# Optimization experiments

Hardware: AMD Instinct MI355X
Metric: run time of the kernel (lower is better)

Reference implementation:

```python
import jax, jax.numpy as jnp
import numpy as np

N_NODES = 50000
N_EDGES = 500000
EDGE_DIM = 16
DIM = 128          # num_features == hidden == 128 so all layers share shapes
N_LAYERS = 3
N_GRAPHS = 512
N_CLASSES = 10
BN_EPS = 1e-5


def _bn(x, g, b, rm, rv):
    # eval-mode BatchNorm1d
    return (x - rm) * jax.lax.rsqrt(rv + BN_EPS) * g + b


def setup_inputs() -> dict:
    key = jax.random.key(0)
    ks = jax.random.split(key, 32)
    s = 0.05
    inp = {
        "x": jax.random.normal(ks[0], (N_NODES, DIM), jnp.float32),
        "edge_attr": jax.random.normal(ks[1], (N_EDGES, EDGE_DIM), jnp.float32),
        "edge_index": jax.random.randint(ks[2], (2, N_EDGES), 0, N_NODES, jnp.int64),
        "batch": jnp.sort(jax.random.randint(ks[3], (N_NODES,), 0, N_GRAPHS, jnp.int64)),
        # edge encoder params (stacked over layers)
        "ee_w1": jax.random.normal(ks[4], (N_LAYERS, EDGE_DIM, DIM), jnp.float32) * s,
        "ee_b1": jax.random.normal(ks[5], (N_LAYERS, DIM), jnp.float32) * s,
        "ee_w2": jax.random.normal(ks[6], (N_LAYERS, DIM, DIM), jnp.float32) * s,
        "ee_b2": jax.random.normal(ks[7], (N_LAYERS, DIM), jnp.float32) * s,
        "ee_bn_g": 1.0 + 0.1 * jax.random.normal(ks[8], (N_LAYERS, DIM), jnp.float32),
        "ee_bn_b": 0.1 * jax.random.normal(ks[9], (N_LAYERS, DIM), jnp.float32),
        "ee_bn_rm": 0.1 * jax.random.normal(ks[10], (N_LAYERS, DIM), jnp.float32),
        "ee_bn_rv": jax.random.uniform(ks[11], (N_LAYERS, DIM), jnp.float32, 0.5, 1.5),
        # node MLP params (stacked over layers)
        "mlp_w1": jax.random.normal(ks[12], (N_LAYERS, DIM, DIM), jnp.float32) * s,
        "mlp_b1": jax.random.normal(ks[13], (N_LAYERS, DIM), jnp.float32) * s,
        "mlp_w2": jax.random.normal(ks[14], (N_LAYERS, DIM, DIM), jnp.float32) * s,
        "mlp_b2": jax.random.normal(ks[15], (N_LAYERS, DIM), jnp.float32) * s,
        "mlp_bn_g": 1.0 + 0.1 * jax.random.normal(ks[16], (N_LAYERS, DIM), jnp.float32),
        "mlp_bn_b": 0.1 * jax.random.normal(ks[17], (N_LAYERS, DIM), jnp.float32),
        "mlp_bn_rm": 0.1 * jax.random.normal(ks[18], (N_LAYERS, DIM), jnp.float32),
        "mlp_bn_rv": jax.random.uniform(ks[19], (N_LAYERS, DIM), jnp.float32, 0.5, 1.5),
        # readout heads
        "lin1_w": jax.random.normal(ks[20], (DIM, DIM), jnp.float32) * s,
        "lin1_b": jax.random.normal(ks[21], (DIM,), jnp.float32) * s,
        "lin2_w": jax.random.normal(ks[22], (DIM, N_CLASSES), jnp.float32) * s,
        "lin2_b": jax.random.normal(ks[23], (N_CLASSES,), jnp.float32) * s,
    }
    return inp


def _forward(x, edge_attr, ee_w1, ee_b1, ee_w2, ee_b2, ee_bn_g, ee_bn_b, ee_bn_rm, ee_bn_rv,
             mlp_w1, mlp_b1, mlp_w2, mlp_b2, mlp_bn_g, mlp_bn_b, mlp_bn_rm, mlp_bn_rv,
             lin1_w, lin1_b, lin2_w, lin2_b, edge_index, batch):
    src, dst = edge_index[0], edge_index[1]  # x_j gathered from src, aggregated at dst
    n_nodes = x.shape[0]
    for i in range(N_LAYERS):
        # edge encoder: Linear -> ReLU -> Linear -> ReLU -> BN
        e = jax.nn.relu(edge_attr @ ee_w1[i] + ee_b1[i])
        e = jax.nn.relu(e @ ee_w2[i] + ee_b2[i])
        e = _bn(e, ee_bn_g[i], ee_bn_b[i], ee_bn_rm[i], ee_bn_rv[i])
        # message: relu(x_j + edge_emb), aggregate: scatter-add to dst
        msg = jax.nn.relu(x[src] + e)                         # [E, DIM]
        agg = jax.ops.segment_sum(msg, dst, num_segments=n_nodes)
        # mlp(x + agg): Linear -> ReLU -> Linear -> ReLU -> BN
        h = x + agg
        h = jax.nn.relu(h @ mlp_w1[i] + mlp_b1[i])
        h = jax.nn.relu(h @ mlp_w2[i] + mlp_b2[i])
        x = _bn(h, mlp_bn_g[i], mlp_bn_b[i], mlp_bn_rm[i], mlp_bn_rv[i])
    # global mean pool over graphs
    sums = jax.ops.segment_sum(x, batch, num_segments=N_GRAPHS)          # [G, DIM]
    cnts = jax.ops.segment_sum(jnp.ones((n_nodes, 1), x.dtype), batch, num_segments=N_GRAPHS)
    pooled = sums / jnp.maximum(cnts, 1.0)
    h = jax.nn.relu(pooled @ lin1_w + lin1_b)   # dropout off in eval mode
    logits = h @ lin2_w + lin2_b
    return jax.nn.log_softmax(logits, axis=-1)


def reference(x, edge_attr, ee_w1, ee_b1, ee_w2, ee_b2, ee_bn_g, ee_bn_b, ee_bn_rm, ee_bn_rv,
              mlp_w1, mlp_b1, mlp_w2, mlp_b2, mlp_bn_g, mlp_bn_b, mlp_bn_rm, mlp_bn_rv,
              lin1_w, lin1_b, lin2_w, lin2_b, edge_index, batch):
    return _forward(x, edge_attr, ee_w1, ee_b1, ee_w2, ee_b2, ee_bn_g, ee_bn_b, ee_bn_rm, ee_bn_rv,
                    mlp_w1, mlp_b1, mlp_w2, mlp_b2, mlp_bn_g, mlp_bn_b, mlp_bn_rm, mlp_bn_rv,
                    lin1_w, lin1_b, lin2_w, lin2_b, edge_index, batch)
```

## Files before the change

### kernel.cpp

```cpp
#include <hip/hip_runtime.h>

#define N_NODES_C 50000
#define N_EDGES_C 500000
#define EDGE_DIM_C 16
#define DIM_C 128
#define N_LAYERS_C 3
#define N_GRAPHS_C 512
#define N_CLASSES_C 10
#define BN_EPS_C 1e-5f

#define SCAN_NB ((N_NODES_C + 1023) / 1024)

typedef short bf16x8 __attribute__((ext_vector_type(8)));
typedef float f32x4  __attribute__((ext_vector_type(4)));

__device__ inline unsigned cvt_pk_bf16(float a, float b) {
    unsigned r;
    asm("v_cvt_pk_bf16_f32 %0, %1, %2" : "=v"(r) : "v"(a), "v"(b));
    return r;
}
__device__ inline float bf2f(unsigned short h) {
    union { unsigned u; float f; } v; v.u = ((unsigned)h) << 16;
    return v.f;
}

__global__ void hist_kernel(const int* __restrict__ dst, int* __restrict__ cnt)
{
    int e = blockIdx.x * blockDim.x + threadIdx.x;
    if (e < N_EDGES_C) atomicAdd(&cnt[dst[e]], 1);
}

__global__ __launch_bounds__(1024)
void scan1_kernel(const int* __restrict__ cnt, int* __restrict__ incl,
                  int* __restrict__ bsum)
{
    __shared__ int buf[1024];
    int i = blockIdx.x * 1024 + threadIdx.x;
    int v = (i < N_NODES_C) ? cnt[i] : 0;
    buf[threadIdx.x] = v;
    __syncthreads();
    for (int off = 1; off < 1024; off <<= 1) {
        int t = (threadIdx.x >= off) ? buf[threadIdx.x - off] : 0;
        __syncthreads();
        buf[threadIdx.x] += t;
        __syncthreads();
    }
    if (i < N_NODES_C) incl[i] = buf[threadIdx.x];
    if (threadIdx.x == 1023) bsum[blockIdx.x] = buf[1023];
}

__global__ void scan2_kernel(int* __restrict__ bsum)
{
    if (threadIdx.x == 0 && blockIdx.x == 0) {
        int run = 0;
        for (int b = 0; b < SCAN_NB; ++b) { int v = bsum[b]; bsum[b] = run; run += v; }
    }
}

__global__ __launch_bounds__(1024)
void scan3_kernel(const int* __restrict__ cnt, const int* __restrict__ incl,
                  const int* __restrict__ bsum,
                  int* __restrict__ offsets, int* __restrict__ cursor)
{
    int i = blockIdx.x * 1024 + threadIdx.x;
    if (i < N_NODES_C) {
        int inc = incl[i] + bsum[blockIdx.x];
        offsets[i + 1] = inc;
        cursor[i] = inc - cnt[i];
        if (i == 0) offsets[0] = 0;
    }
}

__global__ void scatter_kernel(const int* __restrict__ src,
                               const int* __restrict__ dst,
                               const float* __restrict__ ea,
                               int* __restrict__ cursor,
                               int* __restrict__ srcPerm,
                               unsigned short* __restrict__ eaPermH)
{
    int e = blockIdx.x * blockDim.x + threadIdx.x;
    if (e >= N_EDGES_C) return;
    int pos = atomicAdd(&cursor[dst[e]], 1);
    srcPerm[pos] = src[e];
    const float4* in = (const float4*)&ea[(size_t)e * EDGE_DIM_C];
    float4 a = in[0], b = in[1], c = in[2], d = in[3];
    uint4 lo, hi;
    lo.x = cvt_pk_bf16(a.x, a.y); lo.y = cvt_pk_bf16(a.z, a.w);
    lo.z = cvt_pk_bf16(b.x, b.y); lo.w = cvt_pk_bf16(b.z, b.w);
    hi.x = cvt_pk_bf16(c.x, c.y); hi.y = cvt_pk_bf16(c.z, c.w);
    hi.z = cvt_pk_bf16(d.x, d.y); hi.w = cvt_pk_bf16(d.z, d.w);
    uint4* outp = (uint4*)&eaPermH[(size_t)pos * EDGE_DIM_C];
    outp[0] = lo; outp[1] = hi;
}

__global__ __launch_bounds__(512)
void goff_kernel(const int* __restrict__ batch, int* __restrict__ goff)
{
    int g = threadIdx.x;
    int lo = 0, hi = N_NODES_C;
    while (lo < hi) {
        int mid = (lo + hi) >> 1;
        if (batch[mid] < g) lo = mid + 1; else hi = mid;
    }
    goff[g] = lo;
    if (g == 0) goff[N_GRAPHS_C] = N_NODES_C;
}

__global__ __launch_bounds__(256)
void wprep_kernel(const float* __restrict__ ee_w1, const float* __restrict__ ee_w2,
                  const float* __restrict__ mlp_w1, const float* __restrict__ mlp_w2,
                  short* __restrict__ W1T, short* __restrict__ W2T,
                  short* __restrict__ MT1, short* __restrict__ MT2)
{
    int b = blockIdx.x;
    int l = b % 3;
    int which = b / 3;
    if (which == 0) {
        const float* in = ee_w1 + l * 16 * 128;
        short* outp = W1T + l * 128 * 16;
        for (int i = threadIdx.x; i < 2048; i += 256) {
            int f = i >> 4, k = i & 15;
            outp[i] = (short)(cvt_pk_bf16(in[k * 128 + f], 0.f) & 0xffff);
        }
    } else {
        const float* in = (which == 1 ? ee_w2 : which == 2 ? mlp_w1 : mlp_w2) + l * 128 * 128;
        short* outp = (which == 1 ? W2T : which == 2 ? MT1 : MT2) + l * 128 * 128;
        for (int i = threadIdx.x; i < 16384; i += 256) {
            int f = i >> 7, k = i & 127;
            outp[i] = (short)(cvt_pk_bf16(in[k * 128 + f], 0.f) & 0xffff);
        }
    }
}

__global__ __launch_bounds__(256)
void emb_mfma(const unsigned short* __restrict__ eaPermH,
              const short* __restrict__ W1T, const float* __restrict__ b1,
              const short* __restrict__ W2T, const float* __restrict__ b2,
              const float* __restrict__ bng, const float* __restrict__ bnb,
              const float* __restrict__ bnrm, const float* __restrict__ bnrv,
              unsigned short* __restrict__ emb, int c0, int chunkN)
{
    __shared__ short t1s[64 * 128];

    const int tid  = threadIdx.x;
    const int lane = tid & 63;
    const int w    = tid >> 6;
    const int ln15 = lane & 15;
    const int g    = lane >> 4;
    const int colbase = w * 32;

    bf16x8 fw1[2], fw2[2][4];
    float b1v[2], b2v[2], scv[2], shv[2];
    #pragma unroll
    for (int ct = 0; ct < 2; ++ct) {
        int f = colbase + ct * 16 + ln15;
        if (g < 2) fw1[ct] = *(const bf16x8*)&W1T[f * 16 + g * 8];
        else       fw1[ct] = (bf16x8){0,0,0,0,0,0,0,0};
        #pragma unroll
        for (int kb = 0; kb < 4; ++kb)
            fw2[ct][kb] = *(const bf16x8*)&W2T[f * 128 + kb * 32 + g * 8];
        b1v[ct] = b1[f]; b2v[ct] = b2[f];
        float sc = bng[f] * rsqrtf(bnrv[f] + BN_EPS_C);
        scv[ct] = sc; shv[ct] = bnb[f] - bnrm[f] * sc;
    }

    const int niter = (chunkN + 63) / 64;
    for (int it = blockIdx.x; it < niter; it += gridDim.x) {
        const int eb = it * 64;

        #pragma unroll
        for (int rt = 0; rt < 4; ++rt) {
            bf16x8 af;
            if (g < 2) {
                int erow = min(eb + rt * 16 + ln15, chunkN - 1);
                af = *(const bf16x8*)&eaPermH[(size_t)(c0 + erow) * EDGE_DIM_C + g * 8];
            } else {
                af = (bf16x8){0,0,0,0,0,0,0,0};
            }
            #pragma unroll
            for (int ct = 0; ct < 2; ++ct) {
                f32x4 a1 = { b1v[ct], b1v[ct], b1v[ct], b1v[ct] };
                a1 = __builtin_amdgcn_mfma_f32_16x16x32_bf16(af, fw1[ct], a1, 0, 0, 0);
                int col = colbase + ct * 16 + ln15;
                #pragma unroll
                for (int r = 0; r < 4; ++r) {
                    int row = rt * 16 + g * 4 + r;
                    int idx = (row * 128 + col) ^ ((row & 15) << 3);
                    t1s[idx] = (short)(cvt_pk_bf16(fmaxf(a1[r], 0.f), 0.f) & 0xffff);
                }
            }
        }
        __syncthreads();

        f32x4 acc[4][2];
        #pragma unroll
        for (int rt = 0; rt < 4; ++rt)
            #pragma unroll
            for (int ct = 0; ct < 2; ++ct)
                acc[rt][ct] = (f32x4){ b2v[ct], b2v[ct], b2v[ct], b2v[ct] };

        #pragma unroll
        for (int rt = 0; rt < 4; ++rt) {
            bf16x8 a[4];
            int row = rt * 16 + ln15;
            #pragma unroll
            for (int kb = 0; kb < 4; ++kb) {
                int idx = (row * 128 + kb * 32 + g * 8) ^ ((row & 15) << 3);
                a[kb] = *(const bf16x8*)&t1s[idx];
            }
            #pragma unroll
            for (int ct = 0; ct < 2; ++ct)
                #pragma unroll
                for (int kb = 0; kb < 4; ++kb)
                    acc[rt][ct] = __builtin_amdgcn_mfma_f32_16x16x32_bf16(
                        a[kb], fw2[ct][kb], acc[rt][ct], 0, 0, 0);
        }
        __syncthreads();

        #pragma unroll
        for (int rt = 0; rt < 4; ++rt)
            #pragma unroll
            for (int ct = 0; ct < 2; ++ct) {
                int col = colbase + ct * 16 + ln15;
                #pragma unroll
                for (int r = 0; r < 4; ++r) {
                    int row = rt * 16 + g * 4 + r;
                    float v = fmaxf(acc[rt][ct][r], 0.f) * scv[ct] + shv[ct];
                    int idx = (row * 128 + col) ^ ((row & 15) << 3);
                    t1s[idx] = (short)(cvt_pk_bf16(v, 0.f) & 0xffff);
                }
            }
        __syncthreads();

        for (int i = tid; i < 1024; i += 256) {
            int row = i >> 4;
            int c8  = (i & 15) * 8;
            if (eb + row < chunkN) {
                int idx = (row * 128 + c8) ^ ((row & 15) << 3);
                bf16x8 v = *(const bf16x8*)&t1s[idx];
                *(bf16x8*)&emb[(size_t)(eb + row) * 128 + c8] = v;
            }
        }
        __syncthreads();
    }
}

__global__ __launch_bounds__(256)
void agg_kernel(const unsigned short* __restrict__ emb,
                const float* __restrict__ x,
                const int* __restrict__ srcPerm,
                const int* __restrict__ offsets,
                float* __restrict__ agg,
                int c0, int c1, int first)
{
    const int slot = threadIdx.x >> 5;
    const int l    = threadIdx.x & 31;
    const int n = blockIdx.x * 8 + slot;
    if (n >= N_NODES_C) return;

    int lo = offsets[n], hi = offsets[n + 1];
    lo = max(lo, c0); hi = min(hi, c1);

    float4 s = make_float4(0.f, 0.f, 0.f, 0.f);
    const bool any = lo < hi;
    for (int pos = lo; pos < hi; ++pos) {
        int srcn = srcPerm[pos];
        ushort4 eb = *(const ushort4*)&emb[(size_t)(pos - c0) * DIM_C + l * 4];
        float4 xv = *(const float4*)&x[(size_t)srcn * DIM_C + l * 4];
        s.x += fmaxf(xv.x + bf2f(eb.x), 0.f);
        s.y += fmaxf(xv.y + bf2f(eb.y), 0.f);
        s.z += fmaxf(xv.z + bf2f(eb.z), 0.f);
        s.w += fmaxf(xv.w + bf2f(eb.w), 0.f);
    }

    float4* ap = (float4*)&agg[(size_t)n * DIM_C + l * 4];
    if (first) {
        *ap = s;
    } else if (any) {
        float4 o = *ap;
        o.x += s.x; o.y += s.y; o.z += s.z; o.w += s.w;
        *ap = o;
    }
}

__global__ __launch_bounds__(256)
void node_fused(const float* __restrict__ in0, const float* __restrict__ in1,
                const short* __restrict__ WT1, const float* __restrict__ b1,
                const short* __restrict__ WT2, const float* __restrict__ b2,
                const float* __restrict__ bng, const float* __restrict__ bnb,
                const float* __restrict__ bnrm, const float* __restrict__ bnrv,
                float* __restrict__ out, int nrows)
{
    __shared__ short smem[2 * 64 * 128];
    short* hs  = smem;
    short* t1s = smem + 64 * 128;
    float* fout = (float*)smem;

    const int tid  = threadIdx.x;
    const int lane = tid & 63;
    const int w    = tid >> 6;
    const int ln15 = lane & 15;
    const int g    = lane >> 4;
    const int colbase = w * 32;

    bf16x8 fw1[2][4], fw2[2][4];
    float b1v[2], b2v[2], scv[2], shv[2];
    #pragma unroll
    for (int ct = 0; ct < 2; ++ct) {
        int f = colbase + ct * 16 + ln15;
        #pragma unroll
        for (int kb = 0; kb < 4; ++kb) {
            fw1[ct][kb] = *(const bf16x8*)&WT1[f * 128 + kb * 32 + g * 8];
            fw2[ct][kb] = *(const bf16x8*)&WT2[f * 128 + kb * 32 + g * 8];
        }
        b1v[ct] = b1[f]; b2v[ct] = b2[f];
        float sc = bng[f] * rsqrtf(bnrv[f] + BN_EPS_C);
        scv[ct] = sc; shv[ct] = bnb[f] - bnrm[f] * sc;
    }

    const int ntiles = (nrows + 63) / 64;
    for (int t = blockIdx.x; t < ntiles; t += gridDim.x) {
        const int base = t * 64;

        for (int i = tid; i < 2048; i += 256) {
            int row = i >> 5;
            int c4  = (i & 31) * 4;
            int rr  = min(base + row, nrows - 1);
            float4 v = *(const float4*)&in0[(size_t)rr * DIM_C + c4];
            float4 a1 = *(const float4*)&in1[(size_t)rr * DIM_C + c4];
            v.x += a1.x; v.y += a1.y; v.z += a1.z; v.w += a1.w;
            int idx = (row * 128 + c4) ^ ((row & 15) << 3);
            *(unsigned*)&hs[idx]     = cvt_pk_bf16(v.x, v.y);
            *(unsigned*)&hs[idx + 2] = cvt_pk_bf16(v.z, v.w);
        }
        __syncthreads();

        #pragma unroll
        for (int rt = 0; rt < 4; ++rt) {
            bf16x8 a[4];
            int row = rt * 16 + ln15;
            #pragma unroll
            for (int kb = 0; kb < 4; ++kb) {
                int idx = (row * 128 + kb * 32 + g * 8) ^ ((row & 15) << 3);
                a[kb] = *(const bf16x8*)&hs[idx];
            }
            #pragma unroll
            for (int ct = 0; ct < 2; ++ct) {
                f32x4 a1 = { b1v[ct], b1v[ct], b1v[ct], b1v[ct] };
                #pragma unroll
                for (int kb = 0; kb < 4; ++kb)
                    a1 = __builtin_amdgcn_mfma_f32_16x16x32_bf16(a[kb], fw1[ct][kb], a1, 0, 0, 0);
                int col = colbase + ct * 16 + ln15;
                #pragma unroll
                for (int r = 0; r < 4; ++r) {
                    int orow = rt * 16 + g * 4 + r;
                    int idx = (orow * 128 + col) ^ ((orow & 15) << 3);
                    t1s[idx] = (short)(cvt_pk_bf16(fmaxf(a1[r], 0.f), 0.f) & 0xffff);
                }
            }
        }
        __syncthreads();

        f32x4 acc[4][2];
        #pragma unroll
        for (int rt = 0; rt < 4; ++rt)
            #pragma unroll
            for (int ct = 0; ct < 2; ++ct)
                acc[rt][ct] = (f32x4){ b2v[ct], b2v[ct], b2v[ct], b2v[ct] };

        #pragma unroll
        for (int rt = 0; rt < 4; ++rt) {
            bf16x8 a[4];
            int row = rt * 16 + ln15;
            #pragma unroll
            for (int kb = 0; kb < 4; ++kb) {
                int idx = (row * 128 + kb * 32 + g * 8) ^ ((row & 15) << 3);
                a[kb] = *(const bf16x8*)&t1s[idx];
            }
            #pragma unroll
            for (int ct = 0; ct < 2; ++ct)
                #pragma unroll
                for (int kb = 0; kb < 4; ++kb)
                    acc[rt][ct] = __builtin_amdgcn_mfma_f32_16x16x32_bf16(
                        a[kb], fw2[ct][kb], acc[rt][ct], 0, 0, 0);
        }
        __syncthreads();

        #pragma unroll
        for (int rt = 0; rt < 4; ++rt)
            #pragma unroll
            for (int ct = 0; ct < 2; ++ct) {
                int col = colbase + ct * 16 + ln15;
                #pragma unroll
                for (int r = 0; r < 4; ++r) {
                    int row = rt * 16 + g * 4 + r;
                    float v = fmaxf(acc[rt][ct][r], 0.f) * scv[ct] + shv[ct];
                    fout[(row * 128 + col) ^ ((row & 15) << 2)] = v;
                }
            }
        __syncthreads();

        for (int i = tid; i < 2048; i += 256) {
            int row = i >> 5;
            int c4  = (i & 31) * 4;
            int orow = base + row;
            if (orow < nrows) {
                int idx = (row * 128 + c4) ^ ((row & 15) << 2);
                float4 v = *(const float4*)&fout[idx];
                *(float4*)&out[(size_t)orow * DIM_C + c4] = v;
            }
        }
        __syncthreads();
    }
}

__global__ __launch_bounds__(128)
void pool2_kernel(const float* __restrict__ x,
                  const int* __restrict__ goff,
                  float* __restrict__ pooled)
{
    const int g = blockIdx.x;
    const int tid = threadIdx.x;
    int lo = goff[g], hi = goff[g + 1];
    float s = 0.f;
    for (int n = lo; n < hi; ++n)
        s += x[(size_t)n * DIM_C + tid];
    float c = (float)max(hi - lo, 1);
    pooled[g * DIM_C + tid] = s / c;
}

__global__ __launch_bounds__(128)
void head_kernel(const float* __restrict__ pooled,
                 const float* __restrict__ l1w,
                 const float* __restrict__ l1b,
                 const float* __restrict__ l2w,
                 const float* __restrict__ l2b,
                 float* __restrict__ out)
{
    const int g = blockIdx.x;
    const int tid = threadIdx.x;
    __shared__ float ps[DIM_C];
    __shared__ float hsx[DIM_C];
    __shared__ float lg[N_CLASSES_C];
    __shared__ float lse;

    ps[tid] = pooled[g * DIM_C + tid];
    __syncthreads();

    float a = l1b[tid];
    for (int k = 0; k < DIM_C; ++k)
        a += ps[k] * l1w[k * DIM_C + tid];
    hsx[tid] = fmaxf(a, 0.f);
    __syncthreads();

    if (tid < N_CLASSES_C) {
        float s = l2b[tid];
        for (int f = 0; f < DIM_C; ++f)
            s += hsx[f] * l2w[f * N_CLASSES_C + tid];
        lg[tid] = s;
    }
    __syncthreads();

    if (tid == 0) {
        float m = lg[0];
        for (int cc = 1; cc < N_CLASSES_C; ++cc) m = fmaxf(m, lg[cc]);
        float s = 0.f;
        for (int cc = 0; cc < N_CLASSES_C; ++cc) s += expf(lg[cc] - m);
        lse = m + logf(s);
    }
    __syncthreads();

    if (tid < N_CLASSES_C)
        out[g * N_CLASSES_C + tid] = lg[tid] - lse;
}

extern "C" void kernel_launch(void* const* d_in, const int* in_sizes, int n_in,
                              void* d_out, int out_size, void* d_ws, size_t ws_size,
                              hipStream_t stream)
{
    const float* x         = (const float*)d_in[0];
    const float* edge_attr = (const float*)d_in[1];
    const int*   ei        = (const int*)d_in[2];
    const int*   batch     = (const int*)d_in[3];
    const float* ee_w1     = (const float*)d_in[4];
    const float* ee_b1     = (const float*)d_in[5];
    const float* ee_w2     = (const float*)d_in[6];
    const float* ee_b2     = (const float*)d_in[7];
    const float* ee_bn_g   = (const float*)d_in[8];
    const float* ee_bn_b   = (const float*)d_in[9];
    const float* ee_bn_rm  = (const float*)d_in[10];
    const float* ee_bn_rv  = (const float*)d_in[11];
    const float* mlp_w1    = (const float*)d_in[12];
    const float* mlp_b1    = (const float*)d_in[13];
    const float* mlp_w2    = (const float*)d_in[14];
    const float* mlp_b2    = (const float*)d_in[15];
    const float* mlp_bn_g  = (const float*)d_in[16];
    const float* mlp_bn_b  = (const float*)d_in[17];
    const float* mlp_bn_rm = (const float*)d_in[18];
    const float* mlp_bn_rv = (const float*)d_in[19];
    const float* lin1_w    = (const float*)d_in[20];
    const float* lin1_b    = (const float*)d_in[21];
    const float* lin2_w    = (const float*)d_in[22];
    const float* lin2_b    = (const float*)d_in[23];
    float* out = (float*)d_out;

    const int* src = ei;
    const int* dst = ei + N_EDGES_C;

    char* wsp = (char*)d_ws;
    float* x_cur = (float*)wsp;          wsp += (size_t)N_NODES_C * DIM_C * 4;
    float* agg   = (float*)wsp;          wsp += (size_t)N_NODES_C * DIM_C * 4;
    unsigned short* eaPermH = (unsigned short*)wsp;
                                         wsp += (size_t)N_EDGES_C * EDGE_DIM_C * 2;
    int* srcPerm = (int*)wsp;            wsp += (size_t)N_EDGES_C * 4;
    int* cnt     = (int*)wsp;            wsp += 200704;
    int* offsets = (int*)wsp;            wsp += 200704;
    int* cursor  = (int*)wsp;            wsp += 200704;
    int* incl    = (int*)wsp;            wsp += 200704;
    int* bsum    = (int*)wsp;            wsp += 4096;
    int* goff    = (int*)wsp;            wsp += 4096;
    float* pooled = (float*)wsp;         wsp += (size_t)N_GRAPHS_C * DIM_C * 4;
    short* W1T   = (short*)wsp;          wsp += (size_t)N_LAYERS_C * 128 * 16 * 2;
    short* W2T   = (short*)wsp;          wsp += (size_t)N_LAYERS_C * 128 * 128 * 2;
    short* MT1   = (short*)wsp;          wsp += (size_t)N_LAYERS_C * 128 * 128 * 2;
    short* MT2   = (short*)wsp;          wsp += (size_t)N_LAYERS_C * 128 * 128 * 2;
    unsigned short* emb = (unsigned short*)wsp;

    size_t used = (size_t)(wsp - (char*)d_ws);
    size_t embRows = (ws_size > used) ? (ws_size - used) / ((size_t)DIM_C * 2) : 0;
    int chunk = (int)((embRows < (size_t)N_EDGES_C) ? embRows : (size_t)N_EDGES_C);
    if (chunk < 128) chunk = 128;

    wprep_kernel<<<12, 256, 0, stream>>>(ee_w1, ee_w2, mlp_w1, mlp_w2,
                                         W1T, W2T, MT1, MT2);
    hipMemsetAsync(cnt, 0, N_NODES_C * sizeof(int), stream);
    hist_kernel<<<(N_EDGES_C + 255) / 256, 256, 0, stream>>>(dst, cnt);
    scan1_kernel<<<SCAN_NB, 1024, 0, stream>>>(cnt, incl, bsum);
    scan2_kernel<<<1, 64, 0, stream>>>(bsum);
    scan3_kernel<<<SCAN_NB, 1024, 0, stream>>>(cnt, incl, bsum, offsets, cursor);
    scatter_kernel<<<(N_EDGES_C + 255) / 256, 256, 0, stream>>>(
        src, dst, edge_attr, cursor, srcPerm, eaPermH);
    goff_kernel<<<1, 512, 0, stream>>>(batch, goff);

    const float* xin = x;
    for (int i = 0; i < N_LAYERS_C; ++i) {
        for (int c0 = 0; c0 < N_EDGES_C; c0 += chunk) {
            int c1 = min(c0 + chunk, N_EDGES_C);
            emb_mfma<<<1024, 256, 0, stream>>>(
                eaPermH,
                W1T + (size_t)i * 128 * 16, ee_b1 + i * DIM_C,
                W2T + (size_t)i * 128 * 128, ee_b2 + i * DIM_C,
                ee_bn_g + i * DIM_C, ee_bn_b + i * DIM_C,
                ee_bn_rm + i * DIM_C, ee_bn_rv + i * DIM_C,
                emb, c0, c1 - c0);
            agg_kernel<<<(N_NODES_C + 7) / 8, 256, 0, stream>>>(
                emb, xin, srcPerm, offsets, agg, c0, c1, c0 == 0 ? 1 : 0);
        }
        node_fused<<<782, 256, 0, stream>>>(
            xin, agg,
            MT1 + (size_t)i * 128 * 128, mlp_b1 + i * DIM_C,
            MT2 + (size_t)i * 128 * 128, mlp_b2 + i * DIM_C,
            mlp_bn_g + i * DIM_C, mlp_bn_b + i * DIM_C,
            mlp_bn_rm + i * DIM_C, mlp_bn_rv + i * DIM_C,
            x_cur, N_NODES_C);
        xin = x_cur;
    }

    pool2_kernel<<<N_GRAPHS_C, 128, 0, stream>>>(xin, goff, pooled);
    head_kernel<<<N_GRAPHS_C, 128, 0, stream>>>(pooled, lin1_w, lin1_b,
                                                lin2_w, lin2_b, out);
}
```

Measured before the change: 551.0 us.

## Fuse edge aggregation into node MLP kernel with per-tile LDS accumulation

Adds a node_agg_fused kernel that, for each 64-node tile, walks that tile's CSR edge range with 8 groups of 32 threads. It accumulates relu(x_src + emb) in LDS using run-length atomics keyed on a new dstPerm array, then runs the two-layer MLP and BatchNorm. This removes the separate agg kernel and the global round-trip of the aggregated tensor, and ping-pongs the output buffers because the input is read while the output is written. It also raises the emb_mfma grid from 1024 to 1280. The costs are LDS atomics, a larger LDS footprint that may cut occupancy, and an extra dstPerm write and read.

```diff
diff --git a/kernel.cpp b/kernel.cpp
--- a/kernel.cpp
+++ b/kernel.cpp
@@ -76,19 +76,22 @@
                                const float* __restrict__ ea,
                                int* __restrict__ cursor,
                                int* __restrict__ srcPerm,
+                               int* __restrict__ dstPerm,
                                unsigned short* __restrict__ eaPermH)
 {
     int e = blockIdx.x * blockDim.x + threadIdx.x;
     if (e >= N_EDGES_C) return;
-    int pos = atomicAdd(&cursor[dst[e]], 1);
+    int d = dst[e];
+    int pos = atomicAdd(&cursor[d], 1);
     srcPerm[pos] = src[e];
+    dstPerm[pos] = d;
     const float4* in = (const float4*)&ea[(size_t)e * EDGE_DIM_C];
-    float4 a = in[0], b = in[1], c = in[2], d = in[3];
+    float4 a = in[0], b = in[1], c = in[2], dd = in[3];
     uint4 lo, hi;
     lo.x = cvt_pk_bf16(a.x, a.y); lo.y = cvt_pk_bf16(a.z, a.w);
     lo.z = cvt_pk_bf16(b.x, b.y); lo.w = cvt_pk_bf16(b.z, b.w);
     hi.x = cvt_pk_bf16(c.x, c.y); hi.y = cvt_pk_bf16(c.z, c.w);
-    hi.z = cvt_pk_bf16(d.x, d.y); hi.w = cvt_pk_bf16(d.z, d.w);
+    hi.z = cvt_pk_bf16(dd.x, dd.y); hi.w = cvt_pk_bf16(dd.z, dd.w);
     uint4* outp = (uint4*)&eaPermH[(size_t)pos * EDGE_DIM_C];
     outp[0] = lo; outp[1] = hi;
 }
@@ -280,6 +283,184 @@
         float4 o = *ap;
         o.x += s.x; o.y += s.y; o.z += s.z; o.w += s.w;
         *ap = o;
+    }
+}
+
+__global__ __launch_bounds__(256)
+void node_agg_fused(const float* __restrict__ xin,
+                    const unsigned short* __restrict__ emb,
+                    const int* __restrict__ srcPerm,
+                    const int* __restrict__ dstPerm,
+                    const int* __restrict__ offsets,
+                    const short* __restrict__ WT1, const float* __restrict__ b1,
+                    const short* __restrict__ WT2, const float* __restrict__ b2,
+                    const float* __restrict__ bng, const float* __restrict__ bnb,
+                    const float* __restrict__ bnrm, const float* __restrict__ bnrv,
+                    float* __restrict__ out, int nrows)
+{
+    __shared__ float accum[64 * 128];
+    __shared__ short hs[64 * 128];
+    short* t1s = (short*)accum;
+    float* fout = accum;
+
+    const int tid  = threadIdx.x;
+    const int lane = tid & 63;
+    const int w    = tid >> 6;
+    const int ln15 = lane & 15;
+    const int g    = lane >> 4;
+    const int colbase = w * 32;
+
+    bf16x8 fw1[2][4], fw2[2][4];
+    float b1v[2], b2v[2], scv[2], shv[2];
+    #pragma unroll
+    for (int ct = 0; ct < 2; ++ct) {
+        int f = colbase + ct * 16 + ln15;
+        #pragma unroll
+        for (int kb = 0; kb < 4; ++kb) {
+            fw1[ct][kb] = *(const bf16x8*)&WT1[f * 128 + kb * 32 + g * 8];
+            fw2[ct][kb] = *(const bf16x8*)&WT2[f * 128 + kb * 32 + g * 8];
+        }
+        b1v[ct] = b1[f]; b2v[ct] = b2[f];
+        float sc = bng[f] * rsqrtf(bnrv[f] + BN_EPS_C);
+        scv[ct] = sc; shv[ct] = bnb[f] - bnrm[f] * sc;
+    }
+
+    const int ntiles = (nrows + 63) / 64;
+    for (int t = blockIdx.x; t < ntiles; t += gridDim.x) {
+        const int base = t * 64;
+        const int nodeHi = min(base + 64, nrows);
+
+        for (int i = tid; i < 2048; i += 256)
+            *(f32x4*)&accum[i * 4] = (f32x4){0.f, 0.f, 0.f, 0.f};
+        __syncthreads();
+
+        {
+            const int lo = offsets[base];
+            const int hi = offsets[nodeHi];
+            const int g8 = tid >> 5;
+            const int l  = tid & 31;
+            float4 run = make_float4(0.f, 0.f, 0.f, 0.f);
+            int curDst = -1;
+            for (int pos = lo + g8; pos < hi; pos += 8) {
+                int d = dstPerm[pos];
+                if (d != curDst) {
+                    if (curDst >= 0) {
+                        float* ap = &accum[(curDst - base) * 128 + l * 4];
+                        atomicAdd(ap + 0, run.x);
+                        atomicAdd(ap + 1, run.y);
+                        atomicAdd(ap + 2, run.z);
+                        atomicAdd(ap + 3, run.w);
+                    }
+                    curDst = d;
+                    run = make_float4(0.f, 0.f, 0.f, 0.f);
+                }
+                int s = srcPerm[pos];
+                ushort4 e4 = *(const ushort4*)&emb[(size_t)pos * DIM_C + l * 4];
+                float4 xv = *(const float4*)&xin[(size_t)s * DIM_C + l * 4];
+                run.x += fmaxf(xv.x + bf2f(e4.x), 0.f);
+                run.y += fmaxf(xv.y + bf2f(e4.y), 0.f);
+                run.z += fmaxf(xv.z + bf2f(e4.z), 0.f);
+                run.w += fmaxf(xv.w + bf2f(e4.w), 0.f);
+            }
+            if (curDst >= 0) {
+                float* ap = &accum[(curDst - base) * 128 + l * 4];
+                atomicAdd(ap + 0, run.x);
+                atomicAdd(ap + 1, run.y);
+                atomicAdd(ap + 2, run.z);
+                atomicAdd(ap + 3, run.w);
+            }
+        }
+        __syncthreads();
+
+        for (int i = tid; i < 2048; i += 256) {
+            int row = i >> 5;
+            int c4  = (i & 31) * 4;
+            int rr  = min(base + row, nrows - 1);
+            float4 v = *(const float4*)&xin[(size_t)rr * DIM_C + c4];
+            float4 a1 = *(const float4*)&accum[row * 128 + c4];
+            v.x += a1.x; v.y += a1.y; v.z += a1.z; v.w += a1.w;
+            int idx = (row * 128 + c4) ^ ((row & 15) << 3);
+            *(unsigned*)&hs[idx]     = cvt_pk_bf16(v.x, v.y);
+            *(unsigned*)&hs[idx + 2] = cvt_pk_bf16(v.z, v.w);
+        }
+        __syncthreads();
+
+        #pragma unroll
+        for (int rt = 0; rt < 4; ++rt) {
+            bf16x8 a[4];
+            int row = rt * 16 + ln15;
+            #pragma unroll
+            for (int kb = 0; kb < 4; ++kb) {
+                int idx = (row * 128 + kb * 32 + g * 8) ^ ((row & 15) << 3);
+                a[kb] = *(const bf16x8*)&hs[idx];
+            }
+            #pragma unroll
+            for (int ct = 0; ct < 2; ++ct) {
+                f32x4 a1 = { b1v[ct], b1v[ct], b1v[ct], b1v[ct] };
+                #pragma unroll
+                for (int kb = 0; kb < 4; ++kb)
+                    a1 = __builtin_amdgcn_mfma_f32_16x16x32_bf16(a[kb], fw1[ct][kb], a1, 0, 0, 0);
+                int col = colbase + ct * 16 + ln15;
+                #pragma unroll
+                for (int r = 0; r < 4; ++r) {
+                    int orow = rt * 16 + g * 4 + r;
+                    int idx = (orow * 128 + col) ^ ((orow & 15) << 3);
+                    t1s[idx] = (short)(cvt_pk_bf16(fmaxf(a1[r], 0.f), 0.f) & 0xffff);
+                }
+            }
+        }
+        __syncthreads();
+
+        f32x4 acc[4][2];
+        #pragma unroll
+        for (int rt = 0; rt < 4; ++rt)
+            #pragma unroll
+            for (int ct = 0; ct < 2; ++ct)
+                acc[rt][ct] = (f32x4){ b2v[ct], b2v[ct], b2v[ct], b2v[ct] };
+
+        #pragma unroll
+        for (int rt = 0; rt < 4; ++rt) {
+            bf16x8 a[4];
+            int row = rt * 16 + ln15;
+            #pragma unroll
+            for (int kb = 0; kb < 4; ++kb) {
+                int idx = (row * 128 + kb * 32 + g * 8) ^ ((row & 15) << 3);
+                a[kb] = *(const bf16x8*)&t1s[idx];
+            }
+            #pragma unroll
+            for (int ct = 0; ct < 2; ++ct)
+                #pragma unroll
+                for (int kb = 0; kb < 4; ++kb)
+                    acc[rt][ct] = __builtin_amdgcn_mfma_f32_16x16x32_bf16(
+                        a[kb], fw2[ct][kb], acc[rt][ct], 0, 0, 0);
+        }
+        __syncthreads();
+
+        #pragma unroll
+        for (int rt = 0; rt < 4; ++rt)
+            #pragma unroll
+            for (int ct = 0; ct < 2; ++ct) {
+                int col = colbase + ct * 16 + ln15;
+                #pragma unroll
+                for (int r = 0; r < 4; ++r) {
+                    int row = rt * 16 + g * 4 + r;
+                    float v = fmaxf(acc[rt][ct][r], 0.f) * scv[ct] + shv[ct];
+                    fout[(row * 128 + col) ^ ((row & 15) << 2)] = v;
+                }
+            }
+        __syncthreads();
+
+        for (int i = tid; i < 2048; i += 256) {
+            int row = i >> 5;
+            int c4  = (i & 31) * 4;
+            int orow = base + row;
+            if (orow < nrows) {
+                int idx = (row * 128 + c4) ^ ((row & 15) << 2);
+                float4 v = *(const float4*)&fout[idx];
+                *(float4*)&out[(size_t)orow * DIM_C + c4] = v;
+            }
+        }
+        __syncthreads();
     }
 }
 
@@ -509,10 +690,11 @@
 
     char* wsp = (char*)d_ws;
     float* x_cur = (float*)wsp;          wsp += (size_t)N_NODES_C * DIM_C * 4;
-    float* agg   = (float*)wsp;          wsp += (size_t)N_NODES_C * DIM_C * 4;
+    float* aggF  = (float*)wsp;          wsp += (size_t)N_NODES_C * DIM_C * 4;
     unsigned short* eaPermH = (unsigned short*)wsp;
                                          wsp += (size_t)N_EDGES_C * EDGE_DIM_C * 2;
     int* srcPerm = (int*)wsp;            wsp += (size_t)N_EDGES_C * 4;
+    int* dstPerm = (int*)wsp;            wsp += (size_t)N_EDGES_C * 4;
     int* cnt     = (int*)wsp;            wsp += 200704;
     int* offsets = (int*)wsp;            wsp += 200704;
     int* cursor  = (int*)wsp;            wsp += 200704;
@@ -530,6 +712,7 @@
     size_t embRows = (ws_size > used) ? (ws_size - used) / ((size_t)DIM_C * 2) : 0;
     int chunk = (int)((embRows < (size_t)N_EDGES_C) ? embRows : (size_t)N_EDGES_C);
     if (chunk < 128) chunk = 128;
+    const bool fullChunk = (chunk >= N_EDGES_C);
 
     wprep_kernel<<<12, 256, 0, stream>>>(ee_w1, ee_w2, mlp_w1, mlp_w2,
                                          W1T, W2T, MT1, MT2);
@@ -539,34 +722,54 @@
     scan2_kernel<<<1, 64, 0, stream>>>(bsum);
     scan3_kernel<<<SCAN_NB, 1024, 0, stream>>>(cnt, incl, bsum, offsets, cursor);
     scatter_kernel<<<(N_EDGES_C + 255) / 256, 256, 0, stream>>>(
-        src, dst, edge_attr, cursor, srcPerm, eaPermH);
+        src, dst, edge_attr, cursor, srcPerm, dstPerm, eaPermH);
     goff_kernel<<<1, 512, 0, stream>>>(batch, goff);
 
-    const float* xin = x;
+    const float* cur = x;
+    float* bufs[2] = { x_cur, aggF };
     for (int i = 0; i < N_LAYERS_C; ++i) {
-        for (int c0 = 0; c0 < N_EDGES_C; c0 += chunk) {
-            int c1 = min(c0 + chunk, N_EDGES_C);
-            emb_mfma<<<1024, 256, 0, stream>>>(
+        if (fullChunk) {
+            emb_mfma<<<1280, 256, 0, stream>>>(
                 eaPermH,
                 W1T + (size_t)i * 128 * 16, ee_b1 + i * DIM_C,
                 W2T + (size_t)i * 128 * 128, ee_b2 + i * DIM_C,
                 ee_bn_g + i * DIM_C, ee_bn_b + i * DIM_C,
                 ee_bn_rm + i * DIM_C, ee_bn_rv + i * DIM_C,
-                emb, c0, c1 - c0);
-            agg_kernel<<<(N_NODES_C + 7) / 8, 256, 0, stream>>>(
-                emb, xin, srcPerm, offsets, agg, c0, c1, c0 == 0 ? 1 : 0);
-        }
-        node_fused<<<782, 256, 0, stream>>>(
-            xin, agg,
-            MT1 + (size_t)i * 128 * 128, mlp_b1 + i * DIM_C,
-            MT2 + (size_t)i * 128 * 128, mlp_b2 + i * DIM_C,
-            mlp_bn_g + i * DIM_C, mlp_bn_b + i * DIM_C,
-            mlp_bn_rm + i * DIM_C, mlp_bn_rv + i * DIM_C,
-            x_cur, N_NODES_C);
-        xin = x_cur;
-    }
-
-    pool2_kernel<<<N_GRAPHS_C, 128, 0, stream>>>(xin, goff, pooled);
+                emb, 0, N_EDGES_C);
+            float* outp = bufs[i & 1];
+            node_agg_fused<<<768, 256, 0, stream>>>(
+                cur, emb, srcPerm, dstPerm, offsets,
+                MT1 + (size_t)i * 128 * 128, mlp_b1 + i * DIM_C,
+                MT2 + (size_t)i * 128 * 128, mlp_b2 + i * DIM_C,
+                mlp_bn_g + i * DIM_C, mlp_bn_b + i * DIM_C,
+                mlp_bn_rm + i * DIM_C, mlp_bn_rv + i * DIM_C,
+                outp, N_NODES_C);
+            cur = outp;
+        } else {
+            for (int c0 = 0; c0 < N_EDGES_C; c0 += chunk) {
+                int c1 = min(c0 + chunk, N_EDGES_C);
+                emb_mfma<<<1280, 256, 0, stream>>>(
+                    eaPermH,
+                    W1T + (size_t)i * 128 * 16, ee_b1 + i * DIM_C,
+                    W2T + (size_t)i * 128 * 128, ee_b2 + i * DIM_C,
+                    ee_bn_g + i * DIM_C, ee_bn_b + i * DIM_C,
+                    ee_bn_rm + i * DIM_C, ee_bn_rv + i * DIM_C,
+                    emb, c0, c1 - c0);
+                agg_kernel<<<(N_NODES_C + 7) / 8, 256, 0, stream>>>(
+                    emb, cur, srcPerm, offsets, aggF, c0, c1, c0 == 0 ? 1 : 0);
+            }
+            node_fused<<<782, 256, 0, stream>>>(
+                cur, aggF,
+                MT1 + (size_t)i * 128 * 128, mlp_b1 + i * DIM_C,
+                MT2 + (size_t)i * 128 * 128, mlp_b2 + i * DIM_C,
+                mlp_bn_g + i * DIM_C, mlp_bn_b + i * DIM_C,
+                mlp_bn_rm + i * DIM_C, mlp_bn_rv + i * DIM_C,
+                x_cur, N_NODES_C);
+            cur = x_cur;
+        }
+    }
+
+    pool2_kernel<<<N_GRAPHS_C, 128, 0, stream>>>(cur, goff, pooled);
     head_kernel<<<N_GRAPHS_C, 128, 0, stream>>>(pooled, lin1_w, lin1_b,
                                                 lin2_w, lin2_b, out);
 }
```

Result: slower. 1.329 ms (+141.2%).
